# Performance work log

Measured on AMD Instinct MI355X. Metric: run time of the kernel, lower is better.

Reference implementation:

```python
import jax, jax.numpy as jnp
import numpy as np

N = 50000      # nodes
E = 800000     # edges (avg degree 16)
EMB = 128      # emb_dim
NF = 7         # x_features
EF = 5         # edge_features
L = 5          # num_layer
BN_EPS = 1e-5


def setup_inputs() -> dict:
    key = jax.random.key(0)
    ks = jax.random.split(key, 12)
    s = 0.05
    return {
        "x": jax.random.normal(ks[0], (N, NF), jnp.float32),
        "edge_attr": jax.random.normal(ks[1], (E, EF), jnp.float32),
        "edge_index": jax.random.randint(ks[2], (2, E), 0, N, dtype=jnp.int32),
        "W_x": jax.random.normal(ks[3], (NF, EMB), jnp.float32) * s,
        "b_x": jax.random.normal(ks[4], (NF, EMB), jnp.float32) * s,
        "W_e": jax.random.normal(ks[5], (L, EF, EMB), jnp.float32) * s,
        "b_e": jax.random.normal(ks[6], (L, EF, EMB), jnp.float32) * s,
        # per-layer GIN update MLP: Linear(EMB,2EMB)-ReLU-Linear(2EMB,EMB)
        "W1": jax.random.normal(ks[7], (L, EMB, 2 * EMB), jnp.float32) * s,
        "b1": jnp.zeros((L, 2 * EMB), jnp.float32),
        "W2": jax.random.normal(ks[8], (L, 2 * EMB, EMB), jnp.float32) * s,
        "b2": jnp.zeros((L, EMB), jnp.float32),
        # per-layer BatchNorm1d affine params
        "gamma": jnp.ones((L, EMB), jnp.float32),
        "beta": jnp.zeros((L, EMB), jnp.float32),
    }


def reference(x, edge_attr, W_x, b_x, W_e, b_e, W1, b1, W2, b2, gamma, beta, edge_index):
    src, dst = edge_index[0], edge_index[1]
    # initial node embedding: sum of 7 Linear(1,EMB) applied per column == x @ W_x + sum(biases)
    h = x @ W_x + b_x.sum(axis=0)  # [N, EMB]
    for l in range(L):
        # edge embeddings: sum of EF Linear(1,EMB) over edge_attr columns
        e_emb = edge_attr @ W_e[l] + b_e[l].sum(axis=0)  # [E, EMB]
        sl_emb = b_e[l].sum(axis=0)  # self-loop edges have zero attr -> bias sum
        # message = x_j + edge_emb, aggr = add (scatter over dst); self loops add h + sl_emb
        msg = h[src] + e_emb                                        # [E, EMB]
        agg = jax.ops.segment_sum(msg, dst, num_segments=N) + h + sl_emb  # [N, EMB]
        # GIN update MLP
        z = jax.nn.relu(agg @ W1[l] + b1[l]) @ W2[l] + b2[l]        # [N, EMB]
        # BatchNorm1d (training-mode batch stats, biased variance)
        mu = z.mean(axis=0)
        var = z.var(axis=0)
        z = (z - mu) * jax.lax.rsqrt(var + BN_EPS) * gamma[l] + beta[l]
        # ELU on all but last layer; dropout is identity at drop_ratio=0; JK='last'
        h = jax.nn.elu(z) if l < L - 1 else z
    return h
```

## Files before the change

### kernel.cpp

```cpp
#include <hip/hip_runtime.h>
#include <math.h>

#define NN 50000
#define NE 800000
#define EMB 128
#define HID 256
#define NF 7
#define EF 5
#define NL 5
#define BN_EPS 1e-5f
#define NREP 32
#define SCAN_B 196

typedef __attribute__((ext_vector_type(8))) short bf16x8;
typedef __attribute__((ext_vector_type(4))) float f32x4;

__device__ inline unsigned short f2b(float f) {
    unsigned u = __builtin_bit_cast(unsigned, f);
    return (unsigned short)((u + 0x7fffu + ((u >> 16) & 1u)) >> 16);
}
__device__ inline float b2f(unsigned us) {
    return __builtin_bit_cast(float, us << 16);
}
__device__ inline void split2(float a, float b, unsigned& hi, unsigned& lo) {
    unsigned short ha = f2b(a), hb = f2b(b);
    unsigned short la = f2b(a - b2f(ha)), lb = f2b(b - b2f(hb));
    hi = (unsigned)ha | ((unsigned)hb << 16);
    lo = (unsigned)la | ((unsigned)lb << 16);
}
__device__ inline unsigned pkh2(float a, float b) {
    union { unsigned v; _Float16 h[2]; } x;
    x.h[0] = (_Float16)a; x.h[1] = (_Float16)b;
    return x.v;
}
__device__ inline float2 uph2(unsigned u) {
    union { unsigned v; _Float16 h[2]; } x; x.v = u;
    return make_float2((float)x.h[0], (float)x.h[1]);
}

__global__ void k_prep(const float* __restrict__ b_x, const float* __restrict__ b_e,
                       float* __restrict__ bsum_x, float* __restrict__ bsum_e,
                       int* __restrict__ counts, int* __restrict__ cursor) {
    int tid = threadIdx.x;
    if (blockIdx.x == 0 && tid < EMB) {
        float s = 0.f;
        for (int f = 0; f < NF; ++f) s += b_x[f * EMB + tid];
        bsum_x[tid] = s;
        for (int l = 0; l < NL; ++l) {
            float se = 0.f;
            for (int f = 0; f < EF; ++f) se += b_e[(l * EF + f) * EMB + tid];
            bsum_e[l * EMB + tid] = se;
        }
    }
    int gid = blockIdx.x * blockDim.x + tid;
    int stride = gridDim.x * blockDim.x;
    for (int i = gid; i < NN; i += stride) { counts[i] = 0; cursor[i] = 0; }
}

__global__ void k_prepw(const float* __restrict__ W1, const float* __restrict__ W2,
                        unsigned short* __restrict__ W1ph, unsigned short* __restrict__ W1pl,
                        unsigned short* __restrict__ W2ph, unsigned short* __restrict__ W2pl) {
    const int TOT = NL * EMB * HID;
    int gid = blockIdx.x * blockDim.x + threadIdx.x;
    if (gid < TOT) {
        int l = gid / (EMB * HID);
        int r = gid % (EMB * HID);
        int w = r >> 13;
        int rem = r & 8191;
        int h2 = rem >> 11;
        int rem2 = rem & 2047;
        int kk = rem2 >> 9;
        int rem3 = rem2 & 511;
        int lane = rem3 >> 3;
        int j = rem3 & 7;
        int hc = w * 64 + h2 * 16 + (lane & 15);
        int k = kk * 32 + (lane >> 4) * 8 + j;
        float wv = W1[((size_t)l * EMB + k) * HID + hc];
        unsigned short hi = f2b(wv);
        W1ph[gid] = hi;
        W1pl[gid] = f2b(wv - b2f(hi));
    } else if (gid < 2 * TOT) {
        int g = gid - TOT;
        int l = g / (EMB * HID);
        int r = g % (EMB * HID);
        int w = r >> 13;
        int rem = r & 8191;
        int o2 = rem >> 12;
        int rem2 = rem & 4095;
        int kk = rem2 >> 9;
        int rem3 = rem2 & 511;
        int lane = rem3 >> 3;
        int j = rem3 & 7;
        int oc = w * 32 + o2 * 16 + (lane & 15);
        int k2 = kk * 32 + (lane >> 4) * 8 + j;
        float wv = W2[((size_t)l * HID + k2) * EMB + oc];
        unsigned short hi = f2b(wv);
        W2ph[g] = hi;
        W2pl[g] = f2b(wv - b2f(hi));
    }
}

__global__ void k_init(const float* __restrict__ x, const float* __restrict__ W_x,
                       const float* __restrict__ bsum_x, unsigned short* __restrict__ h16) {
    int gid = blockIdx.x * blockDim.x + threadIdx.x;
    int v = gid >> 5;
    if (v >= NN) return;
    int c = (gid & 31) << 2;
    float4 acc = *(const float4*)(bsum_x + c);
    #pragma unroll
    for (int f = 0; f < NF; ++f) {
        float xv = x[(size_t)v * NF + f];
        float4 w = *(const float4*)(W_x + f * EMB + c);
        acc.x += xv * w.x; acc.y += xv * w.y; acc.z += xv * w.z; acc.w += xv * w.w;
    }
    uint2 p = make_uint2(pkh2(acc.x, acc.y), pkh2(acc.z, acc.w));
    *(uint2*)(h16 + (size_t)v * EMB + c) = p;
}

__global__ void k_hist(const int* __restrict__ dst, int* __restrict__ counts) {
    int e = blockIdx.x * blockDim.x + threadIdx.x;
    if (e < NE) atomicAdd(&counts[dst[e]], 1);
}

__global__ void k_scan1(const int* __restrict__ counts, int* __restrict__ bsum) {
    int tid = threadIdx.x;
    int i = blockIdx.x * 256 + tid;
    int v = (i < NN) ? counts[i] : 0;
    #pragma unroll
    for (int off = 1; off < 64; off <<= 1) v += __shfl_xor(v, off, 64);
    __shared__ int ws[4];
    if ((tid & 63) == 0) ws[tid >> 6] = v;
    __syncthreads();
    if (tid == 0) bsum[blockIdx.x] = ws[0] + ws[1] + ws[2] + ws[3];
}

__global__ void k_scan2(const int* __restrict__ bsum, int* __restrict__ bpre,
                        int* __restrict__ row_start) {
    int tid = threadIdx.x;
    int x = (tid < SCAN_B) ? bsum[tid] : 0;
    int lane = tid & 63, wv = tid >> 6;
    int v = x;
    #pragma unroll
    for (int off = 1; off < 64; off <<= 1) {
        int t = __shfl_up(v, off, 64);
        if (lane >= off) v += t;
    }
    __shared__ int wsum[4];
    if (lane == 63) wsum[wv] = v;
    __syncthreads();
    int woff = 0;
    #pragma unroll
    for (int w = 0; w < 4; ++w) if (w < wv) woff += wsum[w];
    int incl = v + woff;
    if (tid < SCAN_B) bpre[tid] = incl - x;
    if (tid == 255) row_start[NN] = incl;
}

__global__ void k_scan3(const int* __restrict__ counts, const int* __restrict__ bpre,
                        int* __restrict__ row_start) {
    int tid = threadIdx.x;
    int i = blockIdx.x * 256 + tid;
    int x = (i < NN) ? counts[i] : 0;
    int lane = tid & 63, wv = tid >> 6;
    int v = x;
    #pragma unroll
    for (int off = 1; off < 64; off <<= 1) {
        int t = __shfl_up(v, off, 64);
        if (lane >= off) v += t;
    }
    __shared__ int wsum[4];
    if (lane == 63) wsum[wv] = v;
    __syncthreads();
    int woff = 0;
    #pragma unroll
    for (int w = 0; w < 4; ++w) if (w < wv) woff += wsum[w];
    if (i < NN) row_start[i] = bpre[blockIdx.x] + v + woff - x;
}

__global__ void k_fill(const int* __restrict__ src, const int* __restrict__ dst,
                       const float* __restrict__ edge_attr,
                       const int* __restrict__ row_start, int* __restrict__ cursor,
                       uint4* __restrict__ sorted_pk) {
    int e = blockIdx.x * blockDim.x + threadIdx.x;
    if (e >= NE) return;
    int d = dst[e];
    int pos = atomicAdd(&cursor[d], 1);
    int idx = row_start[d] + pos;
    const float* ea = edge_attr + (size_t)e * EF;
    float a0 = ea[0], a1 = ea[1], a2 = ea[2], a3 = ea[3], a4 = ea[4];
    uint4 pk;
    pk.x = (unsigned)src[e];
    pk.y = pkh2(a0, a1);
    pk.z = pkh2(a2, a3);
    pk.w = pkh2(a4, 0.f);
    sorted_pk[idx] = pk;
}

__global__ void k_esum(const uint4* __restrict__ sorted_pk,
                       const int* __restrict__ row_start,
                       float* __restrict__ attsum, int* __restrict__ sorted_srcc) {
    int v = blockIdx.x * blockDim.x + threadIdx.x;
    if (v >= NN) return;
    int e0 = row_start[v], e1 = row_start[v + 1];
    float s0 = 0.f, s1 = 0.f, s2 = 0.f, s3 = 0.f, s4 = 0.f;
    for (int e = e0; e < e1; ++e) {
        uint4 pk = sorted_pk[e];
        sorted_srcc[e] = (int)pk.x;
        float2 a01 = uph2(pk.y), a23 = uph2(pk.z), a4x = uph2(pk.w);
        s0 += a01.x; s1 += a01.y; s2 += a23.x; s3 += a23.y; s4 += a4x.x;
    }
    float* o = attsum + (size_t)v * 8;
    *(float4*)(o) = make_float4(s0, s1, s2, s3);
    *(float4*)(o + 4) = make_float4(s4, (float)(e1 - e0), 0.f, 0.f);
}

__global__ __launch_bounds__(256) void k_agg(
        const unsigned short* __restrict__ h16, const int* __restrict__ sorted_srcc,
        const float* __restrict__ attsum,
        const float* __restrict__ W_e_l, const float* __restrict__ bsum_e_l,
        const int* __restrict__ row_start,
        unsigned* __restrict__ agg_hi, unsigned* __restrict__ agg_lo,
        float* __restrict__ stats) {
    int tid = threadIdx.x;
    if (blockIdx.x < NREP) stats[blockIdx.x * 2 * EMB + tid] = 0.f;
    int gid = blockIdx.x * 256 + tid;
    int v = gid >> 6;
    if (v >= NN) return;
    int c = (gid & 63) << 1;
    float2 we0 = *(const float2*)(W_e_l + 0 * EMB + c);
    float2 we1 = *(const float2*)(W_e_l + 1 * EMB + c);
    float2 we2 = *(const float2*)(W_e_l + 2 * EMB + c);
    float2 we3 = *(const float2*)(W_e_l + 3 * EMB + c);
    float2 we4 = *(const float2*)(W_e_l + 4 * EMB + c);
    float2 bs = *(const float2*)(bsum_e_l + c);
    float2 hv = uph2(*(const unsigned*)(h16 + (size_t)v * EMB + c));
    const float* at = attsum + (size_t)v * 8;
    float4 a03 = *(const float4*)(at);
    float2 a45 = *(const float2*)(at + 4);
    float ax = hv.x + (a45.y + 1.f) * bs.x
             + a03.x*we0.x + a03.y*we1.x + a03.z*we2.x + a03.w*we3.x + a45.x*we4.x;
    float ay = hv.y + (a45.y + 1.f) * bs.y
             + a03.x*we0.y + a03.y*we1.y + a03.z*we2.y + a03.w*we3.y + a45.x*we4.y;
    int e0 = row_start[v], e1 = row_start[v + 1];
    int e = e0;
    for (; e + 4 <= e1; e += 4) {
        int s0 = __builtin_amdgcn_readfirstlane(sorted_srcc[e + 0]);
        int s1 = __builtin_amdgcn_readfirstlane(sorted_srcc[e + 1]);
        int s2 = __builtin_amdgcn_readfirstlane(sorted_srcc[e + 2]);
        int s3 = __builtin_amdgcn_readfirstlane(sorted_srcc[e + 3]);
        unsigned u0 = *(const unsigned*)(h16 + (size_t)s0 * EMB + c);
        unsigned u1 = *(const unsigned*)(h16 + (size_t)s1 * EMB + c);
        unsigned u2 = *(const unsigned*)(h16 + (size_t)s2 * EMB + c);
        unsigned u3 = *(const unsigned*)(h16 + (size_t)s3 * EMB + c);
        float2 h0 = uph2(u0), h1 = uph2(u1), h2 = uph2(u2), h3 = uph2(u3);
        ax += (h0.x + h1.x) + (h2.x + h3.x);
        ay += (h0.y + h1.y) + (h2.y + h3.y);
    }
    for (; e < e1; ++e) {
        int s = __builtin_amdgcn_readfirstlane(sorted_srcc[e]);
        float2 hs = uph2(*(const unsigned*)(h16 + (size_t)s * EMB + c));
        ax += hs.x;
        ay += hs.y;
    }
    unsigned phi, plo;
    split2(ax, ay, phi, plo);
    size_t o = (size_t)v * (EMB / 2) + (c >> 1);
    agg_hi[o] = phi;
    agg_lo[o] = plo;
}

__global__ __launch_bounds__(256) void k_mlp(
        const unsigned short* __restrict__ aggh, const unsigned short* __restrict__ aggl,
        const unsigned short* __restrict__ W1ph, const unsigned short* __restrict__ W1pl,
        const float* __restrict__ b1_l,
        const unsigned short* __restrict__ W2ph, const unsigned short* __restrict__ W2pl,
        const float* __restrict__ b2_l,
        unsigned short* __restrict__ z16, float* __restrict__ stats) {
    __shared__ unsigned short Ahi[32][136];
    __shared__ unsigned short Alo[32][136];
    __shared__ unsigned short Hhi[32][264];
    __shared__ unsigned short Hlo[32][264];
    int tid = threadIdx.x;
    int r0 = blockIdx.x * 32;
    int rep = blockIdx.x & (NREP - 1);
    #pragma unroll
    for (int it = 0; it < 4; ++it) {
        int idx = it * 256 + tid;
        int plane = idx >> 9;
        int k = idx & 511;
        int row = k >> 4;
        int cb = (k & 15) * 8;
        int grow = r0 + row;
        uint4 val = make_uint4(0u, 0u, 0u, 0u);
        const unsigned short* srcp = plane ? aggl : aggh;
        if (grow < NN) val = *(const uint4*)(srcp + (size_t)grow * EMB + cb);
        if (plane) *(uint4*)(&Alo[row][cb]) = val;
        else       *(uint4*)(&Ahi[row][cb]) = val;
    }
    __syncthreads();
    int wave = tid >> 6, lane = tid & 63;
    int l16 = lane & 15, quad = lane >> 4;
    {
        bf16x8 ahi[2][4], alo[2][4];
        #pragma unroll
        for (int nt = 0; nt < 2; ++nt)
            #pragma unroll
            for (int kk = 0; kk < 4; ++kk) {
                ahi[nt][kk] = *(const bf16x8*)(&Ahi[nt * 16 + l16][kk * 32 + quad * 8]);
                alo[nt][kk] = *(const bf16x8*)(&Alo[nt * 16 + l16][kk * 32 + quad * 8]);
            }
        #pragma unroll
        for (int h2 = 0; h2 < 4; ++h2) {
            bf16x8 whi[4], wlo[4];
            #pragma unroll
            for (int kk = 0; kk < 4; ++kk) {
                size_t off = ((((size_t)(wave * 4 + h2) * 4) + kk) * 64 + lane) * 8;
                whi[kk] = *(const bf16x8*)(W1ph + off);
                wlo[kk] = *(const bf16x8*)(W1pl + off);
            }
            float4 bv = *(const float4*)(b1_l + wave * 64 + h2 * 16 + quad * 4);
            f32x4 bias = {bv.x, bv.y, bv.z, bv.w};
            #pragma unroll
            for (int nt = 0; nt < 2; ++nt) {
                f32x4 acc = bias;
                #pragma unroll
                for (int kk = 0; kk < 4; ++kk)
                    acc = __builtin_amdgcn_mfma_f32_16x16x32_bf16(whi[kk], ahi[nt][kk], acc, 0, 0, 0);
                #pragma unroll
                for (int kk = 0; kk < 4; ++kk)
                    acc = __builtin_amdgcn_mfma_f32_16x16x32_bf16(whi[kk], alo[nt][kk], acc, 0, 0, 0);
                #pragma unroll
                for (int kk = 0; kk < 4; ++kk)
                    acc = __builtin_amdgcn_mfma_f32_16x16x32_bf16(wlo[kk], ahi[nt][kk], acc, 0, 0, 0);
                float v0 = fmaxf(acc[0], 0.f), v1 = fmaxf(acc[1], 0.f);
                float v2 = fmaxf(acc[2], 0.f), v3 = fmaxf(acc[3], 0.f);
                unsigned hiA, loA, hiB, loB;
                split2(v0, v1, hiA, loA);
                split2(v2, v3, hiB, loB);
                int col = wave * 64 + h2 * 16 + quad * 4;
                *(uint2*)(&Hhi[nt * 16 + l16][col]) = make_uint2(hiA, hiB);
                *(uint2*)(&Hlo[nt * 16 + l16][col]) = make_uint2(loA, loB);
            }
        }
    }
    __syncthreads();
    float ss[2][4] = {}, sq[2][4] = {};
    #pragma unroll
    for (int o2 = 0; o2 < 2; ++o2) {
        bf16x8 w2h[8], w2l[8];
        #pragma unroll
        for (int kk = 0; kk < 8; ++kk) {
            size_t off = ((((size_t)(wave * 2 + o2) * 8) + kk) * 64 + lane) * 8;
            w2h[kk] = *(const bf16x8*)(W2ph + off);
            w2l[kk] = *(const bf16x8*)(W2pl + off);
        }
        float4 bv = *(const float4*)(b2_l + wave * 32 + o2 * 16 + quad * 4);
        f32x4 bias = {bv.x, bv.y, bv.z, bv.w};
        #pragma unroll
        for (int nt = 0; nt < 2; ++nt) {
            bf16x8 hh[8], hl[8];
            #pragma unroll
            for (int kk = 0; kk < 8; ++kk) {
                hh[kk] = *(const bf16x8*)(&Hhi[nt * 16 + l16][kk * 32 + quad * 8]);
                hl[kk] = *(const bf16x8*)(&Hlo[nt * 16 + l16][kk * 32 + quad * 8]);
            }
            f32x4 acc = bias;
            #pragma unroll
            for (int kk = 0; kk < 8; ++kk)
                acc = __builtin_amdgcn_mfma_f32_16x16x32_bf16(w2h[kk], hh[kk], acc, 0, 0, 0);
            #pragma unroll
            for (int kk = 0; kk < 8; ++kk)
                acc = __builtin_amdgcn_mfma_f32_16x16x32_bf16(w2h[kk], hl[kk], acc, 0, 0, 0);
            #pragma unroll
            for (int kk = 0; kk < 8; ++kk)
                acc = __builtin_amdgcn_mfma_f32_16x16x32_bf16(w2l[kk], hh[kk], acc, 0, 0, 0);
            int node = r0 + nt * 16 + l16;
            if (node < NN) {
                uint2 p = make_uint2(pkh2(acc[0], acc[1]), pkh2(acc[2], acc[3]));
                *(uint2*)(z16 + (size_t)node * EMB + wave * 32 + o2 * 16 + quad * 4) = p;
                #pragma unroll
                for (int r = 0; r < 4; ++r) {
                    ss[o2][r] += acc[r];
                    sq[o2][r] += acc[r] * acc[r];
                }
            }
        }
    }
    #pragma unroll
    for (int o2 = 0; o2 < 2; ++o2)
        #pragma unroll
        for (int r = 0; r < 4; ++r) {
            float s = ss[o2][r], q = sq[o2][r];
            #pragma unroll
            for (int m = 1; m < 16; m <<= 1) {
                s += __shfl_xor(s, m, 64);
                q += __shfl_xor(q, m, 64);
            }
            if (l16 == 0) {
                int oc = wave * 32 + o2 * 16 + quad * 4 + r;
                atomicAdd(&stats[rep * 2 * EMB + oc], s);
                atomicAdd(&stats[rep * 2 * EMB + EMB + oc], q);
            }
        }
}

__global__ void k_bnscale(const float* __restrict__ stats,
                          const float* __restrict__ gamma_l, const float* __restrict__ beta_l,
                          float* __restrict__ scsh) {
    int tid = threadIdx.x;
    float s = 0.f, q = 0.f;
    #pragma unroll
    for (int r = 0; r < NREP; ++r) {
        s += stats[r * 2 * EMB + tid];
        q += stats[r * 2 * EMB + EMB + tid];
    }
    float mu = s * (1.f / NN);
    float var = q * (1.f / NN) - mu * mu;
    float sf = gamma_l[tid] * rsqrtf(var + BN_EPS);
    scsh[tid] = sf;
    scsh[EMB + tid] = beta_l[tid] - mu * sf;
}

__global__ void k_bn(const unsigned short* __restrict__ z16, const float* __restrict__ scsh,
                     unsigned short* __restrict__ h16, float* __restrict__ fout, int last) {
    __shared__ float sc[EMB], sh[EMB];
    int tid = threadIdx.x;
    if (tid < EMB) {
        sc[tid] = scsh[tid];
        sh[tid] = scsh[EMB + tid];
    }
    __syncthreads();
    int gid = blockIdx.x * blockDim.x + tid;
    if (gid >= NN * EMB / 4) return;
    int c = (gid & 31) << 2;
    uint2 zp = *(const uint2*)(z16 + (size_t)gid * 4);
    float2 z01 = uph2(zp.x), z23 = uph2(zp.y);
    float o0 = z01.x * sc[c + 0] + sh[c + 0];
    float o1 = z01.y * sc[c + 1] + sh[c + 1];
    float o2 = z23.x * sc[c + 2] + sh[c + 2];
    float o3 = z23.y * sc[c + 3] + sh[c + 3];
    if (!last) {
        o0 = (o0 > 0.f) ? o0 : (expf(o0) - 1.f);
        o1 = (o1 > 0.f) ? o1 : (expf(o1) - 1.f);
        o2 = (o2 > 0.f) ? o2 : (expf(o2) - 1.f);
        o3 = (o3 > 0.f) ? o3 : (expf(o3) - 1.f);
        uint2 p = make_uint2(pkh2(o0, o1), pkh2(o2, o3));
        *(uint2*)(h16 + (size_t)gid * 4) = p;
    } else {
        *(float4*)(fout + (size_t)gid * 4) = make_float4(o0, o1, o2, o3);
    }
}

extern "C" void kernel_launch(void* const* d_in, const int* in_sizes, int n_in,
                              void* d_out, int out_size, void* d_ws, size_t ws_size,
                              hipStream_t stream) {
    const float* x         = (const float*)d_in[0];
    const float* edge_attr = (const float*)d_in[1];
    const int*   edge_idx  = (const int*)d_in[2];
    const float* W_x   = (const float*)d_in[3];
    const float* b_x   = (const float*)d_in[4];
    const float* W_e   = (const float*)d_in[5];
    const float* b_e   = (const float*)d_in[6];
    const float* W1    = (const float*)d_in[7];
    const float* b1    = (const float*)d_in[8];
    const float* W2    = (const float*)d_in[9];
    const float* b2    = (const float*)d_in[10];
    const float* gamma = (const float*)d_in[11];
    const float* beta  = (const float*)d_in[12];
    float* fout = (float*)d_out;

    const int* src = edge_idx;
    const int* dst = edge_idx + NE;

    char* p = (char*)d_ws;
    auto alloc = [&](size_t bytes) { char* q = p; p += (bytes + 255) & ~(size_t)255; return q; };
    unsigned short* h16 = (unsigned short*)alloc((size_t)NN * EMB * 2);
    unsigned short* z16 = (unsigned short*)alloc((size_t)NN * EMB * 2);
    unsigned* agg_hi = (unsigned*)alloc((size_t)NN * EMB * 2);
    unsigned* agg_lo = (unsigned*)alloc((size_t)NN * EMB * 2);
    unsigned short* W1ph = (unsigned short*)alloc((size_t)NL * HID * EMB * 2);
    unsigned short* W1pl = (unsigned short*)alloc((size_t)NL * HID * EMB * 2);
    unsigned short* W2ph = (unsigned short*)alloc((size_t)NL * EMB * HID * 2);
    unsigned short* W2pl = (unsigned short*)alloc((size_t)NL * EMB * HID * 2);
    int*   row_start  = (int*)alloc((NN + 1) * sizeof(int));
    int*   counts     = (int*)alloc(NN * sizeof(int));
    int*   cursor     = (int*)alloc(NN * sizeof(int));
    uint4* sorted_pk  = (uint4*)alloc((size_t)NE * sizeof(uint4));
    int*   sorted_srcc= (int*)alloc((size_t)NE * sizeof(int));
    float* attsum     = (float*)alloc((size_t)NN * 8 * sizeof(float));
    int*   bsum       = (int*)alloc(SCAN_B * sizeof(int));
    int*   bpre       = (int*)alloc(SCAN_B * sizeof(int));
    float* stats      = (float*)alloc((size_t)NREP * 2 * EMB * sizeof(float));
    float* scsh       = (float*)alloc(2 * EMB * sizeof(float));
    float* bsum_x     = (float*)alloc(EMB * sizeof(float));
    float* bsum_e     = (float*)alloc(NL * EMB * sizeof(float));

    k_prep<<<256, 256, 0, stream>>>(b_x, b_e, bsum_x, bsum_e, counts, cursor);
    k_prepw<<<(2 * NL * EMB * HID + 255) / 256, 256, 0, stream>>>(W1, W2, W1ph, W1pl, W2ph, W2pl);
    k_init<<<(NN * 32 + 255) / 256, 256, 0, stream>>>(x, W_x, bsum_x, h16);
    k_hist<<<(NE + 255) / 256, 256, 0, stream>>>(dst, counts);
    k_scan1<<<SCAN_B, 256, 0, stream>>>(counts, bsum);
    k_scan2<<<1, 256, 0, stream>>>(bsum, bpre, row_start);
    k_scan3<<<SCAN_B, 256, 0, stream>>>(counts, bpre, row_start);
    k_fill<<<(NE + 255) / 256, 256, 0, stream>>>(src, dst, edge_attr, row_start, cursor,
                                                 sorted_pk);
    k_esum<<<SCAN_B, 256, 0, stream>>>(sorted_pk, row_start, attsum, sorted_srcc);
    for (int l = 0; l < NL; ++l) {
        k_agg<<<(NN * 64 + 255) / 256, 256, 0, stream>>>(
            h16, sorted_srcc, attsum, W_e + (size_t)l * EF * EMB, bsum_e + l * EMB,
            row_start, agg_hi, agg_lo, stats);
        k_mlp<<<(NN + 31) / 32, 256, 0, stream>>>(
            (const unsigned short*)agg_hi, (const unsigned short*)agg_lo,
            W1ph + (size_t)l * HID * EMB, W1pl + (size_t)l * HID * EMB, b1 + (size_t)l * HID,
            W2ph + (size_t)l * EMB * HID, W2pl + (size_t)l * EMB * HID, b2 + (size_t)l * EMB,
            z16, stats);
        k_bnscale<<<1, 128, 0, stream>>>(stats, gamma + l * EMB, beta + l * EMB, scsh);
        k_bn<<<(NN * EMB / 4 + 255) / 256, 256, 0, stream>>>(
            z16, scsh, h16, fout, (l == NL - 1) ? 1 : 0);
    }
}
```

Measured before the change: 640.0 us.

## Fuse neighbor aggregation into MLP kernel, writing aggregates directly to LDS

Merges the gather/aggregation kernel into the MLP kernel. Each wave aggregates 8 nodes and writes the hi/lo bf16 split directly to shared memory, so the agg_hi/agg_lo round trip through global memory and one launch per layer go away. Stats zeroing moves to the prep kernel and to bnscale after it reads the sums, and the gather loop is unrolled to 8 edges. The risk is lower parallelism: only 4 waves per 32-row block now do the latency-bound gather, serially over 8 nodes each, and the MMA phase has to wait for them.

```diff
diff --git a/kernel.cpp b/kernel.cpp
--- a/kernel.cpp
+++ b/kernel.cpp
@@ -40,7 +40,8 @@
 
 __global__ void k_prep(const float* __restrict__ b_x, const float* __restrict__ b_e,
                        float* __restrict__ bsum_x, float* __restrict__ bsum_e,
-                       int* __restrict__ counts, int* __restrict__ cursor) {
+                       int* __restrict__ counts, int* __restrict__ cursor,
+                       float* __restrict__ stats) {
     int tid = threadIdx.x;
     if (blockIdx.x == 0 && tid < EMB) {
         float s = 0.f;
@@ -55,6 +56,7 @@
     int gid = blockIdx.x * blockDim.x + tid;
     int stride = gridDim.x * blockDim.x;
     for (int i = gid; i < NN; i += stride) { counts[i] = 0; cursor[i] = 0; }
+    for (int i = gid; i < NREP * 2 * EMB; i += stride) stats[i] = 0.f;
 }
 
 __global__ void k_prepw(const float* __restrict__ W1, const float* __restrict__ W2,
@@ -214,63 +216,11 @@
     *(float4*)(o + 4) = make_float4(s4, (float)(e1 - e0), 0.f, 0.f);
 }
 
-__global__ __launch_bounds__(256) void k_agg(
+__global__ __launch_bounds__(256) void k_aggmlp(
         const unsigned short* __restrict__ h16, const int* __restrict__ sorted_srcc,
         const float* __restrict__ attsum,
         const float* __restrict__ W_e_l, const float* __restrict__ bsum_e_l,
         const int* __restrict__ row_start,
-        unsigned* __restrict__ agg_hi, unsigned* __restrict__ agg_lo,
-        float* __restrict__ stats) {
-    int tid = threadIdx.x;
-    if (blockIdx.x < NREP) stats[blockIdx.x * 2 * EMB + tid] = 0.f;
-    int gid = blockIdx.x * 256 + tid;
-    int v = gid >> 6;
-    if (v >= NN) return;
-    int c = (gid & 63) << 1;
-    float2 we0 = *(const float2*)(W_e_l + 0 * EMB + c);
-    float2 we1 = *(const float2*)(W_e_l + 1 * EMB + c);
-    float2 we2 = *(const float2*)(W_e_l + 2 * EMB + c);
-    float2 we3 = *(const float2*)(W_e_l + 3 * EMB + c);
-    float2 we4 = *(const float2*)(W_e_l + 4 * EMB + c);
-    float2 bs = *(const float2*)(bsum_e_l + c);
-    float2 hv = uph2(*(const unsigned*)(h16 + (size_t)v * EMB + c));
-    const float* at = attsum + (size_t)v * 8;
-    float4 a03 = *(const float4*)(at);
-    float2 a45 = *(const float2*)(at + 4);
-    float ax = hv.x + (a45.y + 1.f) * bs.x
-             + a03.x*we0.x + a03.y*we1.x + a03.z*we2.x + a03.w*we3.x + a45.x*we4.x;
-    float ay = hv.y + (a45.y + 1.f) * bs.y
-             + a03.x*we0.y + a03.y*we1.y + a03.z*we2.y + a03.w*we3.y + a45.x*we4.y;
-    int e0 = row_start[v], e1 = row_start[v + 1];
-    int e = e0;
-    for (; e + 4 <= e1; e += 4) {
-        int s0 = __builtin_amdgcn_readfirstlane(sorted_srcc[e + 0]);
-        int s1 = __builtin_amdgcn_readfirstlane(sorted_srcc[e + 1]);
-        int s2 = __builtin_amdgcn_readfirstlane(sorted_srcc[e + 2]);
-        int s3 = __builtin_amdgcn_readfirstlane(sorted_srcc[e + 3]);
-        unsigned u0 = *(const unsigned*)(h16 + (size_t)s0 * EMB + c);
-        unsigned u1 = *(const unsigned*)(h16 + (size_t)s1 * EMB + c);
-        unsigned u2 = *(const unsigned*)(h16 + (size_t)s2 * EMB + c);
-        unsigned u3 = *(const unsigned*)(h16 + (size_t)s3 * EMB + c);
-        float2 h0 = uph2(u0), h1 = uph2(u1), h2 = uph2(u2), h3 = uph2(u3);
-        ax += (h0.x + h1.x) + (h2.x + h3.x);
-        ay += (h0.y + h1.y) + (h2.y + h3.y);
-    }
-    for (; e < e1; ++e) {
-        int s = __builtin_amdgcn_readfirstlane(sorted_srcc[e]);
-        float2 hs = uph2(*(const unsigned*)(h16 + (size_t)s * EMB + c));
-        ax += hs.x;
-        ay += hs.y;
-    }
-    unsigned phi, plo;
-    split2(ax, ay, phi, plo);
-    size_t o = (size_t)v * (EMB / 2) + (c >> 1);
-    agg_hi[o] = phi;
-    agg_lo[o] = plo;
-}
-
-__global__ __launch_bounds__(256) void k_mlp(
-        const unsigned short* __restrict__ aggh, const unsigned short* __restrict__ aggl,
         const unsigned short* __restrict__ W1ph, const unsigned short* __restrict__ W1pl,
         const float* __restrict__ b1_l,
         const unsigned short* __restrict__ W2ph, const unsigned short* __restrict__ W2pl,
@@ -283,23 +233,67 @@
     int tid = threadIdx.x;
     int r0 = blockIdx.x * 32;
     int rep = blockIdx.x & (NREP - 1);
-    #pragma unroll
-    for (int it = 0; it < 4; ++it) {
-        int idx = it * 256 + tid;
-        int plane = idx >> 9;
-        int k = idx & 511;
-        int row = k >> 4;
-        int cb = (k & 15) * 8;
-        int grow = r0 + row;
-        uint4 val = make_uint4(0u, 0u, 0u, 0u);
-        const unsigned short* srcp = plane ? aggl : aggh;
-        if (grow < NN) val = *(const uint4*)(srcp + (size_t)grow * EMB + cb);
-        if (plane) *(uint4*)(&Alo[row][cb]) = val;
-        else       *(uint4*)(&Ahi[row][cb]) = val;
-    }
-    __syncthreads();
     int wave = tid >> 6, lane = tid & 63;
     int l16 = lane & 15, quad = lane >> 4;
+    {
+        int c = lane << 1;
+        float2 we0 = *(const float2*)(W_e_l + 0 * EMB + c);
+        float2 we1 = *(const float2*)(W_e_l + 1 * EMB + c);
+        float2 we2 = *(const float2*)(W_e_l + 2 * EMB + c);
+        float2 we3 = *(const float2*)(W_e_l + 3 * EMB + c);
+        float2 we4 = *(const float2*)(W_e_l + 4 * EMB + c);
+        float2 bs = *(const float2*)(bsum_e_l + c);
+        #pragma unroll
+        for (int i = 0; i < 8; ++i) {
+            int n = wave * 8 + i;
+            int v = r0 + n;
+            unsigned phi = 0u, plo = 0u;
+            if (v < NN) {
+                float2 hv = uph2(*(const unsigned*)(h16 + (size_t)v * EMB + c));
+                const float* at = attsum + (size_t)v * 8;
+                float4 a03 = *(const float4*)(at);
+                float2 a45 = *(const float2*)(at + 4);
+                float ax = hv.x + (a45.y + 1.f) * bs.x
+                         + a03.x*we0.x + a03.y*we1.x + a03.z*we2.x + a03.w*we3.x + a45.x*we4.x;
+                float ay = hv.y + (a45.y + 1.f) * bs.y
+                         + a03.x*we0.y + a03.y*we1.y + a03.z*we2.y + a03.w*we3.y + a45.x*we4.y;
+                int e0 = row_start[v], e1 = row_start[v + 1];
+                int e = e0;
+                for (; e + 8 <= e1; e += 8) {
+                    int s0 = __builtin_amdgcn_readfirstlane(sorted_srcc[e + 0]);
+                    int s1 = __builtin_amdgcn_readfirstlane(sorted_srcc[e + 1]);
+                    int s2 = __builtin_amdgcn_readfirstlane(sorted_srcc[e + 2]);
+                    int s3 = __builtin_amdgcn_readfirstlane(sorted_srcc[e + 3]);
+                    int s4 = __builtin_amdgcn_readfirstlane(sorted_srcc[e + 4]);
+                    int s5 = __builtin_amdgcn_readfirstlane(sorted_srcc[e + 5]);
+                    int s6 = __builtin_amdgcn_readfirstlane(sorted_srcc[e + 6]);
+                    int s7 = __builtin_amdgcn_readfirstlane(sorted_srcc[e + 7]);
+                    unsigned u0 = *(const unsigned*)(h16 + (size_t)s0 * EMB + c);
+                    unsigned u1 = *(const unsigned*)(h16 + (size_t)s1 * EMB + c);
+                    unsigned u2 = *(const unsigned*)(h16 + (size_t)s2 * EMB + c);
+                    unsigned u3 = *(const unsigned*)(h16 + (size_t)s3 * EMB + c);
+                    unsigned u4 = *(const unsigned*)(h16 + (size_t)s4 * EMB + c);
+                    unsigned u5 = *(const unsigned*)(h16 + (size_t)s5 * EMB + c);
+                    unsigned u6 = *(const unsigned*)(h16 + (size_t)s6 * EMB + c);
+                    unsigned u7 = *(const unsigned*)(h16 + (size_t)s7 * EMB + c);
+                    float2 h0 = uph2(u0), h1 = uph2(u1), h2 = uph2(u2), h3 = uph2(u3);
+                    float2 h4 = uph2(u4), h5 = uph2(u5), h6 = uph2(u6), h7 = uph2(u7);
+                    ax += ((h0.x + h1.x) + (h2.x + h3.x)) + ((h4.x + h5.x) + (h6.x + h7.x));
+                    ay += ((h0.y + h1.y) + (h2.y + h3.y)) + ((h4.y + h5.y) + (h6.y + h7.y));
+                }
+                for (; e < e1; ++e) {
+                    int s = __builtin_amdgcn_readfirstlane(sorted_srcc[e]);
+                    float2 hs = uph2(*(const unsigned*)(h16 + (size_t)s * EMB + c));
+                    ax += hs.x;
+                    ay += hs.y;
+                }
+                split2(ax, ay, phi, plo);
+            }
+            *(unsigned*)(&Ahi[n][c]) = phi;
+            *(unsigned*)(&Alo[n][c]) = plo;
+        }
+    }
+    __syncthreads();
     {
         bf16x8 ahi[2][4], alo[2][4];
         #pragma unroll
@@ -404,7 +398,7 @@
         }
 }
 
-__global__ void k_bnscale(const float* __restrict__ stats,
+__global__ void k_bnscale(float* __restrict__ stats,
                           const float* __restrict__ gamma_l, const float* __restrict__ beta_l,
                           float* __restrict__ scsh) {
     int tid = threadIdx.x;
@@ -414,6 +408,8 @@
         s += stats[r * 2 * EMB + tid];
         q += stats[r * 2 * EMB + EMB + tid];
     }
+    __syncthreads();
+    for (int i = tid; i < NREP * 2 * EMB; i += 128) stats[i] = 0.f;
     float mu = s * (1.f / NN);
     float var = q * (1.f / NN) - mu * mu;
     float sf = gamma_l[tid] * rsqrtf(var + BN_EPS);
@@ -476,8 +472,6 @@
     auto alloc = [&](size_t bytes) { char* q = p; p += (bytes + 255) & ~(size_t)255; return q; };
     unsigned short* h16 = (unsigned short*)alloc((size_t)NN * EMB * 2);
     unsigned short* z16 = (unsigned short*)alloc((size_t)NN * EMB * 2);
-    unsigned* agg_hi = (unsigned*)alloc((size_t)NN * EMB * 2);
-    unsigned* agg_lo = (unsigned*)alloc((size_t)NN * EMB * 2);
     unsigned short* W1ph = (unsigned short*)alloc((size_t)NL * HID * EMB * 2);
     unsigned short* W1pl = (unsigned short*)alloc((size_t)NL * HID * EMB * 2);
     unsigned short* W2ph = (unsigned short*)alloc((size_t)NL * EMB * HID * 2);
@@ -495,7 +489,7 @@
     float* bsum_x     = (float*)alloc(EMB * sizeof(float));
     float* bsum_e     = (float*)alloc(NL * EMB * sizeof(float));
 
-    k_prep<<<256, 256, 0, stream>>>(b_x, b_e, bsum_x, bsum_e, counts, cursor);
+    k_prep<<<256, 256, 0, stream>>>(b_x, b_e, bsum_x, bsum_e, counts, cursor, stats);
     k_prepw<<<(2 * NL * EMB * HID + 255) / 256, 256, 0, stream>>>(W1, W2, W1ph, W1pl, W2ph, W2pl);
     k_init<<<(NN * 32 + 255) / 256, 256, 0, stream>>>(x, W_x, bsum_x, h16);
     k_hist<<<(NE + 255) / 256, 256, 0, stream>>>(dst, counts);
@@ -506,11 +500,9 @@
                                                  sorted_pk);
     k_esum<<<SCAN_B, 256, 0, stream>>>(sorted_pk, row_start, attsum, sorted_srcc);
     for (int l = 0; l < NL; ++l) {
-        k_agg<<<(NN * 64 + 255) / 256, 256, 0, stream>>>(
+        k_aggmlp<<<(NN + 31) / 32, 256, 0, stream>>>(
             h16, sorted_srcc, attsum, W_e + (size_t)l * EF * EMB, bsum_e + l * EMB,
-            row_start, agg_hi, agg_lo, stats);
-        k_mlp<<<(NN + 31) / 32, 256, 0, stream>>>(
-            (const unsigned short*)agg_hi, (const unsigned short*)agg_lo,
+            row_start,
             W1ph + (size_t)l * HID * EMB, W1pl + (size_t)l * HID * EMB, b1 + (size_t)l * HID,
             W2ph + (size_t)l * EMB * HID, W2pl + (size_t)l * EMB * HID, b2 + (size_t)l * EMB,
             z16, stats);
```

Result: slower. 946.8 us (+47.9%).

## Fuse BatchNorm and ELU into the next layer's gather, drop per-layer BN pass

Applied to the files above, without the earlier changes.

The per-layer BN+ELU kernel is removed for layers 0-3. The next layer's aggregation kernel now reads the raw bf16 MLP output, applies the BN scale/shift and ELU on the fly to each gathered neighbour value, and only the final layer runs a standalone BN pass. This removes a full read+write of the node state per layer and four kernel launches, but recomputes the affine+exp on every gathered edge (about 16x redundant) and uses the fast __expf. The gather loop is also unrolled from 4 to 8 neighbours for more memory-level parallelism.

```diff
diff --git a/kernel.cpp b/kernel.cpp
--- a/kernel.cpp
+++ b/kernel.cpp
@@ -214,9 +214,10 @@
     *(float4*)(o + 4) = make_float4(s4, (float)(e1 - e0), 0.f, 0.f);
 }
 
+template<int APPLY_BN>
 __global__ __launch_bounds__(256) void k_agg(
-        const unsigned short* __restrict__ h16, const int* __restrict__ sorted_srcc,
-        const float* __restrict__ attsum,
+        const unsigned short* __restrict__ st16, const int* __restrict__ sorted_srcc,
+        const float* __restrict__ attsum, const float* __restrict__ scsh,
         const float* __restrict__ W_e_l, const float* __restrict__ bsum_e_l,
         const int* __restrict__ row_start,
         unsigned* __restrict__ agg_hi, unsigned* __restrict__ agg_lo,
@@ -233,7 +234,22 @@
     float2 we3 = *(const float2*)(W_e_l + 3 * EMB + c);
     float2 we4 = *(const float2*)(W_e_l + 4 * EMB + c);
     float2 bs = *(const float2*)(bsum_e_l + c);
-    float2 hv = uph2(*(const unsigned*)(h16 + (size_t)v * EMB + c));
+    float2 sc2 = make_float2(0.f, 0.f), sh2 = make_float2(0.f, 0.f);
+    if (APPLY_BN) {
+        sc2 = *(const float2*)(scsh + c);
+        sh2 = *(const float2*)(scsh + EMB + c);
+    }
+    auto state = [&](unsigned u) -> float2 {
+        float2 t = uph2(u);
+        if (APPLY_BN) {
+            t.x = t.x * sc2.x + sh2.x;
+            t.y = t.y * sc2.y + sh2.y;
+            t.x = (t.x > 0.f) ? t.x : (__expf(t.x) - 1.f);
+            t.y = (t.y > 0.f) ? t.y : (__expf(t.y) - 1.f);
+        }
+        return t;
+    };
+    float2 hv = state(*(const unsigned*)(st16 + (size_t)v * EMB + c));
     const float* at = attsum + (size_t)v * 8;
     float4 a03 = *(const float4*)(at);
     float2 a45 = *(const float2*)(at + 4);
@@ -243,22 +259,31 @@
              + a03.x*we0.y + a03.y*we1.y + a03.z*we2.y + a03.w*we3.y + a45.x*we4.y;
     int e0 = row_start[v], e1 = row_start[v + 1];
     int e = e0;
-    for (; e + 4 <= e1; e += 4) {
+    for (; e + 8 <= e1; e += 8) {
         int s0 = __builtin_amdgcn_readfirstlane(sorted_srcc[e + 0]);
         int s1 = __builtin_amdgcn_readfirstlane(sorted_srcc[e + 1]);
         int s2 = __builtin_amdgcn_readfirstlane(sorted_srcc[e + 2]);
         int s3 = __builtin_amdgcn_readfirstlane(sorted_srcc[e + 3]);
-        unsigned u0 = *(const unsigned*)(h16 + (size_t)s0 * EMB + c);
-        unsigned u1 = *(const unsigned*)(h16 + (size_t)s1 * EMB + c);
-        unsigned u2 = *(const unsigned*)(h16 + (size_t)s2 * EMB + c);
-        unsigned u3 = *(const unsigned*)(h16 + (size_t)s3 * EMB + c);
-        float2 h0 = uph2(u0), h1 = uph2(u1), h2 = uph2(u2), h3 = uph2(u3);
-        ax += (h0.x + h1.x) + (h2.x + h3.x);
-        ay += (h0.y + h1.y) + (h2.y + h3.y);
+        int s4 = __builtin_amdgcn_readfirstlane(sorted_srcc[e + 4]);
+        int s5 = __builtin_amdgcn_readfirstlane(sorted_srcc[e + 5]);
+        int s6 = __builtin_amdgcn_readfirstlane(sorted_srcc[e + 6]);
+        int s7 = __builtin_amdgcn_readfirstlane(sorted_srcc[e + 7]);
+        unsigned u0 = *(const unsigned*)(st16 + (size_t)s0 * EMB + c);
+        unsigned u1 = *(const unsigned*)(st16 + (size_t)s1 * EMB + c);
+        unsigned u2 = *(const unsigned*)(st16 + (size_t)s2 * EMB + c);
+        unsigned u3 = *(const unsigned*)(st16 + (size_t)s3 * EMB + c);
+        unsigned u4 = *(const unsigned*)(st16 + (size_t)s4 * EMB + c);
+        unsigned u5 = *(const unsigned*)(st16 + (size_t)s5 * EMB + c);
+        unsigned u6 = *(const unsigned*)(st16 + (size_t)s6 * EMB + c);
+        unsigned u7 = *(const unsigned*)(st16 + (size_t)s7 * EMB + c);
+        float2 h0 = state(u0), h1 = state(u1), h2 = state(u2), h3 = state(u3);
+        float2 h4 = state(u4), h5 = state(u5), h6 = state(u6), h7 = state(u7);
+        ax += ((h0.x + h1.x) + (h2.x + h3.x)) + ((h4.x + h5.x) + (h6.x + h7.x));
+        ay += ((h0.y + h1.y) + (h2.y + h3.y)) + ((h4.y + h5.y) + (h6.y + h7.y));
     }
     for (; e < e1; ++e) {
         int s = __builtin_amdgcn_readfirstlane(sorted_srcc[e]);
-        float2 hs = uph2(*(const unsigned*)(h16 + (size_t)s * EMB + c));
+        float2 hs = state(*(const unsigned*)(st16 + (size_t)s * EMB + c));
         ax += hs.x;
         ay += hs.y;
     }
@@ -422,7 +447,7 @@
 }
 
 __global__ void k_bn(const unsigned short* __restrict__ z16, const float* __restrict__ scsh,
-                     unsigned short* __restrict__ h16, float* __restrict__ fout, int last) {
+                     float* __restrict__ fout) {
     __shared__ float sc[EMB], sh[EMB];
     int tid = threadIdx.x;
     if (tid < EMB) {
@@ -439,16 +464,7 @@
     float o1 = z01.y * sc[c + 1] + sh[c + 1];
     float o2 = z23.x * sc[c + 2] + sh[c + 2];
     float o3 = z23.y * sc[c + 3] + sh[c + 3];
-    if (!last) {
-        o0 = (o0 > 0.f) ? o0 : (expf(o0) - 1.f);
-        o1 = (o1 > 0.f) ? o1 : (expf(o1) - 1.f);
-        o2 = (o2 > 0.f) ? o2 : (expf(o2) - 1.f);
-        o3 = (o3 > 0.f) ? o3 : (expf(o3) - 1.f);
-        uint2 p = make_uint2(pkh2(o0, o1), pkh2(o2, o3));
-        *(uint2*)(h16 + (size_t)gid * 4) = p;
-    } else {
-        *(float4*)(fout + (size_t)gid * 4) = make_float4(o0, o1, o2, o3);
-    }
+    *(float4*)(fout + (size_t)gid * 4) = make_float4(o0, o1, o2, o3);
 }
 
 extern "C" void kernel_launch(void* const* d_in, const int* in_sizes, int n_in,
@@ -505,17 +521,25 @@
     k_fill<<<(NE + 255) / 256, 256, 0, stream>>>(src, dst, edge_attr, row_start, cursor,
                                                  sorted_pk);
     k_esum<<<SCAN_B, 256, 0, stream>>>(sorted_pk, row_start, attsum, sorted_srcc);
+    const int AGG_GRID = (NN * 64 + 255) / 256;
     for (int l = 0; l < NL; ++l) {
-        k_agg<<<(NN * 64 + 255) / 256, 256, 0, stream>>>(
-            h16, sorted_srcc, attsum, W_e + (size_t)l * EF * EMB, bsum_e + l * EMB,
-            row_start, agg_hi, agg_lo, stats);
+        if (l == 0) {
+            k_agg<0><<<AGG_GRID, 256, 0, stream>>>(
+                h16, sorted_srcc, attsum, scsh,
+                W_e + (size_t)l * EF * EMB, bsum_e + l * EMB, row_start,
+                agg_hi, agg_lo, stats);
+        } else {
+            k_agg<1><<<AGG_GRID, 256, 0, stream>>>(
+                z16, sorted_srcc, attsum, scsh,
+                W_e + (size_t)l * EF * EMB, bsum_e + l * EMB, row_start,
+                agg_hi, agg_lo, stats);
+        }
         k_mlp<<<(NN + 31) / 32, 256, 0, stream>>>(
             (const unsigned short*)agg_hi, (const unsigned short*)agg_lo,
             W1ph + (size_t)l * HID * EMB, W1pl + (size_t)l * HID * EMB, b1 + (size_t)l * HID,
             W2ph + (size_t)l * EMB * HID, W2pl + (size_t)l * EMB * HID, b2 + (size_t)l * EMB,
             z16, stats);
         k_bnscale<<<1, 128, 0, stream>>>(stats, gamma + l * EMB, beta + l * EMB, scsh);
-        k_bn<<<(NN * EMB / 4 + 255) / 256, 256, 0, stream>>>(
-            z16, scsh, h16, fout, (l == NL - 1) ? 1 : 0);
-    }
-}
+    }
+    k_bn<<<(NN * EMB / 4 + 255) / 256, 256, 0, stream>>>(z16, scsh, fout);
+}
```

Result: no change. 634.6 us (-0.8%).
